# Kernel optimization log

Hardware: AMD Instinct MI355X
Metric: run time of the kernel (lower is better)

The kernel has to match this reference:

```python
import jax, jax.numpy as jnp
import numpy as np

HEADS = 4
DIM_HEAD = 32
SCALE = 10.0
EPS = 1e-12  # F.normalize eps


def setup_inputs() -> dict:
    key = jax.random.key(0)
    k0, k1, k2 = jax.random.split(key, 3)
    b, c, h, w = 4, 256, 64, 64
    hidden = HEADS * DIM_HEAD  # 128
    x = jax.random.normal(k0, (b, c, h, w), dtype=jnp.float32)
    # 1x1 convs == per-pixel linear layers; store as [out_ch, in_ch]
    w_qkv = jax.random.normal(k1, (3 * hidden, c), dtype=jnp.float32) * (1.0 / np.sqrt(c))
    w_out = jax.random.normal(k2, (c, hidden), dtype=jnp.float32) * (1.0 / np.sqrt(hidden))
    b_out = jnp.zeros((c,), dtype=jnp.float32)
    return {"x": x, "w_qkv": w_qkv, "w_out": w_out, "b_out": b_out}


def _l2norm(t):
    # normalize along the per-head feature dim d (axis=2 of [b,h,d,n])
    n = jnp.sqrt(jnp.sum(t * t, axis=2, keepdims=True))
    return t / jnp.maximum(n, EPS)


def reference(x, w_qkv, w_out, b_out):
    b, c, h, w = x.shape
    n = h * w
    # to_qkv 1x1 conv (no bias)
    qkv = jnp.einsum('oc,bchw->bohw', w_qkv, x)          # [b, 3*hidden, h, w]
    qkv = qkv.reshape(b, 3, HEADS, DIM_HEAD, n)          # chunk dim=1 then split heads
    q, k, v = qkv[:, 0], qkv[:, 1], qkv[:, 2]            # each [b, heads, d, n]
    q = _l2norm(q)
    k = _l2norm(k)
    sim = jnp.einsum('bhdi,bhdj->bhij', q, k) * SCALE    # [b, heads, n, n]
    attn = jax.nn.softmax(sim, axis=-1)
    out = jnp.einsum('bhij,bhdj->bhid', attn, v)         # [b, heads, n, d]
    # 'b h (x y) d -> b (h d) x y'
    out = out.transpose(0, 1, 3, 2).reshape(b, HEADS * DIM_HEAD, h, w)
    # to_out 1x1 conv with bias
    return jnp.einsum('oc,bchw->bohw', w_out, out) + b_out[None, :, None, None]
```

## Files before the change

### kernel.cpp

```cpp
#include <hip/hip_runtime.h>
#include <math.h>

#define BB 4
#define CC 256
#define NHEAD 4
#define DH 32
#define NN 4096
#define HID 128

typedef _Float16 f16;
typedef _Float16 f16x8 __attribute__((ext_vector_type(8)));
typedef _Float16 f16x4 __attribute__((ext_vector_type(4)));
typedef float f32x4 __attribute__((ext_vector_type(4)));

#define QPRESCALE 14.42695041f
#define NSHIFT 14.42695041f

#if __has_builtin(__builtin_amdgcn_exp2f)
#define EXP2F(x) __builtin_amdgcn_exp2f(x)
#else
#define EXP2F(x) __expf((x)*0.6931471805599453f)
#endif

__device__ __forceinline__ f16x8 cvt8(const float* p) {
    float4 a = *(const float4*)p;
    float4 b = *(const float4*)(p + 4);
    f16x8 r;
    r[0] = (f16)a.x; r[1] = (f16)a.y; r[2] = (f16)a.z; r[3] = (f16)a.w;
    r[4] = (f16)b.x; r[5] = (f16)b.y; r[6] = (f16)b.z; r[7] = (f16)b.w;
    return r;
}

__global__ __launch_bounds__(256) void qkv_fused(const float* __restrict__ x,
                                                 const float* __restrict__ wq,
                                                 f16* __restrict__ qh,
                                                 f16* __restrict__ kh,
                                                 f16* __restrict__ vh) {
    int wave = threadIdx.x >> 6, lane = threadIdx.x & 63;
    int quad = lane >> 4, col = lane & 15;
    int b = blockIdx.z;
    int o0 = blockIdx.y * 64;
    int i0 = blockIdx.x * 128 + wave * 32;
    const float* xb = x + (size_t)b * CC * NN;

    f32x4 c[4][2];
#pragma unroll
    for (int mt = 0; mt < 4; mt++)
#pragma unroll
        for (int nt = 0; nt < 2; nt++) c[mt][nt] = f32x4{0.f, 0.f, 0.f, 0.f};

#pragma unroll
    for (int k0 = 0; k0 < CC; k0 += 32) {
        f16x8 a[4];
#pragma unroll
        for (int mt = 0; mt < 4; mt++)
            a[mt] = cvt8(wq + (size_t)(o0 + mt * 16 + col) * CC + k0 + quad * 8);
#pragma unroll
        for (int nt = 0; nt < 2; nt++) {
            const float* xc = xb + (size_t)(k0 + quad * 8) * NN + i0 + nt * 16 + col;
            f16x8 bf;
#pragma unroll
            for (int j = 0; j < 8; j++) bf[j] = (f16)xc[(size_t)j * NN];
#pragma unroll
            for (int mt = 0; mt < 4; mt++)
                c[mt][nt] = __builtin_amdgcn_mfma_f32_16x16x32_f16(a[mt], bf, c[mt][nt], 0, 0, 0);
        }
    }

    if (o0 < 256) {
        int isQ = (o0 < 128);
        int obase = isQ ? o0 : (o0 - 128);
        f16* dst = isQ ? qh : kh;
        float pre = isQ ? QPRESCALE : 1.0f;
#pragma unroll
        for (int nt = 0; nt < 2; nt++) {
#pragma unroll
            for (int hh = 0; hh < 2; hh++) {
                float ss = 0.f;
#pragma unroll
                for (int m2 = 0; m2 < 2; m2++)
#pragma unroll
                    for (int r = 0; r < 4; r++) {
                        float v = c[hh * 2 + m2][nt][r];
                        ss = fmaf(v, v, ss);
                    }
                ss += __shfl_xor(ss, 16);
                ss += __shfl_xor(ss, 32);
                float inv = pre / fmaxf(sqrtf(ss), 1e-12f);
                int h = (obase + hh * 32) >> 5;
                size_t row = ((size_t)(b * 4 + h) * NN + i0 + nt * 16 + col) * 32;
#pragma unroll
                for (int m2 = 0; m2 < 2; m2++) {
                    f16x4 st;
#pragma unroll
                    for (int r = 0; r < 4; r++) st[r] = (f16)(c[hh * 2 + m2][nt][r] * inv);
                    *(f16x4*)(dst + row + m2 * 16 + quad * 4) = st;
                }
            }
        }
    } else {
        int o2 = o0 - 256;
#pragma unroll
        for (int nt = 0; nt < 2; nt++) {
            int i = i0 + nt * 16 + col;
#pragma unroll
            for (int mt = 0; mt < 4; mt++) {
                int h = (o2 + mt * 16) >> 5;
                int d = (mt & 1) * 16 + quad * 4;
#pragma unroll
                for (int r = 0; r < 4; r++)
                    vh[((size_t)(b * 4 + h) * 32 + d + r) * NN + i] = (f16)c[mt][nt][r];
            }
        }
    }
}

#define KROW 40
#define VROW 72

struct KV32 {
    f16x8 k0, k1;
    f16x4 v0n0, v0n1, v1n0, v1n1;
};

__device__ __forceinline__ KV32 lds_frags(const f16* kl, const f16* vl,
                                          int jb, int col, int quad) {
    KV32 f;
    f.k0 = *(const f16x8*)(kl + (jb + col) * KROW + quad * 8);
    f.k1 = *(const f16x8*)(kl + (jb + 16 + col) * KROW + quad * 8);
    f.v0n0 = *(const f16x4*)(vl + col * VROW + jb + quad * 4);
    f.v0n1 = *(const f16x4*)(vl + (16 + col) * VROW + jb + quad * 4);
    f.v1n0 = *(const f16x4*)(vl + col * VROW + jb + 16 + quad * 4);
    f.v1n1 = *(const f16x4*)(vl + (16 + col) * VROW + jb + 16 + quad * 4);
    return f;
}

__device__ __forceinline__ f16x4 expblk(f32x4 s, float& lacc) {
    float p0 = EXP2F(s[0]), p1 = EXP2F(s[1]);
    float p2 = EXP2F(s[2]), p3 = EXP2F(s[3]);
    lacc += (p0 + p1) + (p2 + p3);
    f16x4 r;
    r[0] = (f16)p0; r[1] = (f16)p1; r[2] = (f16)p2; r[3] = (f16)p3;
    return r;
}

__device__ __forceinline__ void compute32(const KV32& f, f16x8 qB0, f16x8 qB1,
                                          f32x4& o00, f32x4& o01,
                                          f32x4& o10, f32x4& o11,
                                          float& l0, float& l1) {
    const f32x4 zs = {-NSHIFT, -NSHIFT, -NSHIFT, -NSHIFT};
    f32x4 s00 = __builtin_amdgcn_mfma_f32_16x16x32_f16(f.k0, qB0, zs, 0, 0, 0);
    f32x4 s10 = __builtin_amdgcn_mfma_f32_16x16x32_f16(f.k0, qB1, zs, 0, 0, 0);
    f32x4 s01 = __builtin_amdgcn_mfma_f32_16x16x32_f16(f.k1, qB0, zs, 0, 0, 0);
    f32x4 s11 = __builtin_amdgcn_mfma_f32_16x16x32_f16(f.k1, qB1, zs, 0, 0, 0);
    f16x4 p00 = expblk(s00, l0);
    f16x4 p10 = expblk(s10, l1);
    f16x4 p01 = expblk(s01, l0);
    f16x4 p11 = expblk(s11, l1);
    o00 = __builtin_amdgcn_mfma_f32_16x16x16f16(p00, f.v0n0, o00, 0, 0, 0);
    o01 = __builtin_amdgcn_mfma_f32_16x16x16f16(p00, f.v0n1, o01, 0, 0, 0);
    o10 = __builtin_amdgcn_mfma_f32_16x16x16f16(p10, f.v0n0, o10, 0, 0, 0);
    o11 = __builtin_amdgcn_mfma_f32_16x16x16f16(p10, f.v0n1, o11, 0, 0, 0);
    o00 = __builtin_amdgcn_mfma_f32_16x16x16f16(p01, f.v1n0, o00, 0, 0, 0);
    o01 = __builtin_amdgcn_mfma_f32_16x16x16f16(p01, f.v1n1, o01, 0, 0, 0);
    o10 = __builtin_amdgcn_mfma_f32_16x16x16f16(p11, f.v1n0, o10, 0, 0, 0);
    o11 = __builtin_amdgcn_mfma_f32_16x16x16f16(p11, f.v1n1, o11, 0, 0, 0);
}

__global__ __launch_bounds__(256, 4) void attn_mfma(const f16* __restrict__ qh,
                                                    const f16* __restrict__ kh,
                                                    const f16* __restrict__ vh,
                                                    f16* __restrict__ att16) {
    __shared__ __align__(16) f16 klds[2][64 * KROW];
    __shared__ __align__(16) f16 vlds[2][32 * VROW];
    int t = threadIdx.x;
    int wave = t >> 6, lane = t & 63;
    int quad = lane >> 4, col = lane & 15;

    int bid = blockIdx.x;
    int xcd = bid & 7;
    int slot = bid >> 3;
    int bh = xcd * 2 + (slot >> 5);
    int i0 = (slot & 31) * 128;
    int iw = i0 + wave * 32;

    const f16* qb = qh + (size_t)bh * NN * 32;
    const f16* kb = kh + (size_t)bh * NN * 32;
    const f16* vb = vh + (size_t)bh * 32 * NN;

    f16x8 qB0 = *(const f16x8*)(qb + (size_t)(iw + col) * 32 + quad * 8);
    f16x8 qB1 = *(const f16x8*)(qb + (size_t)(iw + 16 + col) * 32 + quad * 8);

    f32x4 o00 = {0.f, 0.f, 0.f, 0.f}, o01 = o00, o10 = o00, o11 = o00;
    float l0 = 0.f, l1 = 0.f;

    int ktr = t >> 2, kts = t & 3;
    int vtr = t >> 3, vts = t & 7;

    f16x8 kr, vr;
    kr = *(const f16x8*)(kb + (size_t)(0 + ktr) * 32 + kts * 8);
    vr = *(const f16x8*)(vb + (size_t)vtr * NN + 0 + vts * 8);
    *(f16x8*)(&klds[0][0] + ktr * KROW + kts * 8) = kr;
    *(f16x8*)(&vlds[0][0] + vtr * VROW + vts * 8) = vr;
    __syncthreads();
    kr = *(const f16x8*)(kb + (size_t)(64 + ktr) * 32 + kts * 8);
    vr = *(const f16x8*)(vb + (size_t)vtr * NN + 64 + vts * 8);

    for (int tile = 0; tile < 62; tile++) {
        int buf = tile & 1;
        const f16* kl = &klds[buf][0];
        const f16* vl = &vlds[buf][0];
        KV32 f0 = lds_frags(kl, vl, 0, col, quad);
        KV32 f1 = lds_frags(kl, vl, 32, col, quad);
        compute32(f0, qB0, qB1, o00, o01, o10, o11, l0, l1);
        compute32(f1, qB0, qB1, o00, o01, o10, o11, l0, l1);
        *(f16x8*)(&klds[buf ^ 1][0] + ktr * KROW + kts * 8) = kr;
        *(f16x8*)(&vlds[buf ^ 1][0] + vtr * VROW + vts * 8) = vr;
        __syncthreads();
        int j0 = (tile + 2) * 64;
        kr = *(const f16x8*)(kb + (size_t)(j0 + ktr) * 32 + kts * 8);
        vr = *(const f16x8*)(vb + (size_t)vtr * NN + j0 + vts * 8);
    }
    {
        KV32 f0 = lds_frags(&klds[0][0], &vlds[0][0], 0, col, quad);
        KV32 f1 = lds_frags(&klds[0][0], &vlds[0][0], 32, col, quad);
        compute32(f0, qB0, qB1, o00, o01, o10, o11, l0, l1);
        compute32(f1, qB0, qB1, o00, o01, o10, o11, l0, l1);
        *(f16x8*)(&klds[1][0] + ktr * KROW + kts * 8) = kr;
        *(f16x8*)(&vlds[1][0] + vtr * VROW + vts * 8) = vr;
        __syncthreads();
    }
    {
        KV32 f0 = lds_frags(&klds[1][0], &vlds[1][0], 0, col, quad);
        KV32 f1 = lds_frags(&klds[1][0], &vlds[1][0], 32, col, quad);
        compute32(f0, qB0, qB1, o00, o01, o10, o11, l0, l1);
        compute32(f1, qB0, qB1, o00, o01, o10, o11, l0, l1);
    }

    l0 += __shfl_xor(l0, 16); l0 += __shfl_xor(l0, 32);
    l1 += __shfl_xor(l1, 16); l1 += __shfl_xor(l1, 32);

    int b = bh >> 2, h = bh & 3;
    f16* ab = att16 + (size_t)b * NN * HID + h * 32;
#pragma unroll
    for (int r = 0; r < 4; r++) {
        float inv0 = __builtin_amdgcn_rcpf(__shfl(l0, quad * 4 + r));
        float inv1 = __builtin_amdgcn_rcpf(__shfl(l1, quad * 4 + r));
        size_t row0 = (size_t)(iw + quad * 4 + r) * HID;
        size_t row1 = (size_t)(iw + 16 + quad * 4 + r) * HID;
        ab[row0 + col]      = (f16)(o00[r] * inv0);
        ab[row0 + 16 + col] = (f16)(o01[r] * inv0);
        ab[row1 + col]      = (f16)(o10[r] * inv1);
        ab[row1 + 16 + col] = (f16)(o11[r] * inv1);
    }
}

__global__ __launch_bounds__(256) void out_mfma(const f16* __restrict__ att16,
                                                const float* __restrict__ wo,
                                                const float* __restrict__ bo,
                                                float* __restrict__ out) {
    int wave = threadIdx.x >> 6, lane = threadIdx.x & 63;
    int quad = lane >> 4, col = lane & 15;
    int b = blockIdx.z;
    int i0 = (blockIdx.x * 4 + wave) * 32;
    int o0 = blockIdx.y * 64;
    const f16* ab = att16 + (size_t)b * NN * HID;

    const f32x4 z = {0.f, 0.f, 0.f, 0.f};
    f32x4 c[2][4];
#pragma unroll
    for (int it = 0; it < 2; it++)
#pragma unroll
        for (int ot = 0; ot < 4; ot++) c[it][ot] = z;

#pragma unroll
    for (int k0 = 0; k0 < HID; k0 += 32) {
        f16x8 a0 = *(const f16x8*)(ab + (size_t)(i0 + col) * HID + k0 + quad * 8);
        f16x8 a1 = *(const f16x8*)(ab + (size_t)(i0 + 16 + col) * HID + k0 + quad * 8);
#pragma unroll
        for (int ot = 0; ot < 4; ot++) {
            f16x8 bf = cvt8(wo + (size_t)(o0 + ot * 16 + col) * HID + k0 + quad * 8);
            c[0][ot] = __builtin_amdgcn_mfma_f32_16x16x32_f16(a0, bf, c[0][ot], 0, 0, 0);
            c[1][ot] = __builtin_amdgcn_mfma_f32_16x16x32_f16(a1, bf, c[1][ot], 0, 0, 0);
        }
    }

#pragma unroll
    for (int it = 0; it < 2; it++)
#pragma unroll
        for (int ot = 0; ot < 4; ot++) {
            int o = o0 + ot * 16 + col;
            float bias = bo[o];
            int i = i0 + it * 16 + quad * 4;
            float4 st = {c[it][ot][0] + bias, c[it][ot][1] + bias,
                         c[it][ot][2] + bias, c[it][ot][3] + bias};
            *(float4*)(out + ((size_t)b * CC + o) * NN + i) = st;
        }
}

extern "C" void kernel_launch(void* const* d_in, const int* in_sizes, int n_in,
                              void* d_out, int out_size, void* d_ws, size_t ws_size,
                              hipStream_t stream) {
    const float* x     = (const float*)d_in[0];
    const float* w_qkv = (const float*)d_in[1];
    const float* w_out = (const float*)d_in[2];
    const float* b_out = (const float*)d_in[3];
    float* out = (float*)d_out;

    char* ws = (char*)d_ws;
    f16* qh    = (f16*)(ws);
    f16* kh    = (f16*)(ws + (4u << 20));
    f16* vh    = (f16*)(ws + (8u << 20));
    f16* att16 = (f16*)(ws + (12u << 20));

    qkv_fused<<<dim3(NN / 128, 384 / 64, BB), 256, 0, stream>>>(x, w_qkv, qh, kh, vh);
    attn_mfma<<<dim3(512), 256, 0, stream>>>(qh, kh, vh, att16);
    out_mfma<<<dim3(NN / 128, CC / 64, BB), 256, 0, stream>>>(att16, w_out, b_out, out);
}
```

Baseline: 167.8 us.

## Retile attention to 16 queries per wave and widen output tiles in projections

The attention kernel now gives each wave 16 query rows instead of 32 and launches 1024 blocks instead of 512. This spreads the dominant attention work over more CUs, but each block reloads the full K/V stream for half as many queries. The QKV and output projection kernels double the output channels per block (128 instead of 64), so each x or att16 fragment load feeds more MFMAs. The cost is more accumulator registers and fewer blocks in those two kernels.

```diff
diff --git a/kernel.cpp b/kernel.cpp
--- a/kernel.cpp
+++ b/kernel.cpp
@@ -39,43 +39,41 @@
     int wave = threadIdx.x >> 6, lane = threadIdx.x & 63;
     int quad = lane >> 4, col = lane & 15;
     int b = blockIdx.z;
-    int o0 = blockIdx.y * 64;
+    int y = blockIdx.y;
+    int o0 = y * 128;
     int i0 = blockIdx.x * 128 + wave * 32;
     const float* xb = x + (size_t)b * CC * NN;
 
-    f32x4 c[4][2];
-#pragma unroll
-    for (int mt = 0; mt < 4; mt++)
+    f32x4 c[8][2];
+#pragma unroll
+    for (int mt = 0; mt < 8; mt++)
 #pragma unroll
         for (int nt = 0; nt < 2; nt++) c[mt][nt] = f32x4{0.f, 0.f, 0.f, 0.f};
 
 #pragma unroll
     for (int k0 = 0; k0 < CC; k0 += 32) {
-        f16x8 a[4];
-#pragma unroll
-        for (int mt = 0; mt < 4; mt++)
-            a[mt] = cvt8(wq + (size_t)(o0 + mt * 16 + col) * CC + k0 + quad * 8);
+        f16x8 bf[2];
 #pragma unroll
         for (int nt = 0; nt < 2; nt++) {
             const float* xc = xb + (size_t)(k0 + quad * 8) * NN + i0 + nt * 16 + col;
-            f16x8 bf;
-#pragma unroll
-            for (int j = 0; j < 8; j++) bf[j] = (f16)xc[(size_t)j * NN];
-#pragma unroll
-            for (int mt = 0; mt < 4; mt++)
-                c[mt][nt] = __builtin_amdgcn_mfma_f32_16x16x32_f16(a[mt], bf, c[mt][nt], 0, 0, 0);
-        }
-    }
-
-    if (o0 < 256) {
-        int isQ = (o0 < 128);
-        int obase = isQ ? o0 : (o0 - 128);
-        f16* dst = isQ ? qh : kh;
-        float pre = isQ ? QPRESCALE : 1.0f;
+#pragma unroll
+            for (int j = 0; j < 8; j++) bf[nt][j] = (f16)xc[(size_t)j * NN];
+        }
+#pragma unroll
+        for (int mt = 0; mt < 8; mt++) {
+            f16x8 a = cvt8(wq + (size_t)(o0 + mt * 16 + col) * CC + k0 + quad * 8);
+            c[mt][0] = __builtin_amdgcn_mfma_f32_16x16x32_f16(a, bf[0], c[mt][0], 0, 0, 0);
+            c[mt][1] = __builtin_amdgcn_mfma_f32_16x16x32_f16(a, bf[1], c[mt][1], 0, 0, 0);
+        }
+    }
+
+    if (y < 2) {
+        f16* dst = (y == 0) ? qh : kh;
+        float pre = (y == 0) ? QPRESCALE : 1.0f;
 #pragma unroll
         for (int nt = 0; nt < 2; nt++) {
 #pragma unroll
-            for (int hh = 0; hh < 2; hh++) {
+            for (int hh = 0; hh < 4; hh++) {
                 float ss = 0.f;
 #pragma unroll
                 for (int m2 = 0; m2 < 2; m2++)
@@ -87,8 +85,7 @@
                 ss += __shfl_xor(ss, 16);
                 ss += __shfl_xor(ss, 32);
                 float inv = pre / fmaxf(sqrtf(ss), 1e-12f);
-                int h = (obase + hh * 32) >> 5;
-                size_t row = ((size_t)(b * 4 + h) * NN + i0 + nt * 16 + col) * 32;
+                size_t row = ((size_t)(b * 4 + hh) * NN + i0 + nt * 16 + col) * 32;
 #pragma unroll
                 for (int m2 = 0; m2 < 2; m2++) {
                     f16x4 st;
@@ -99,13 +96,12 @@
             }
         }
     } else {
-        int o2 = o0 - 256;
 #pragma unroll
         for (int nt = 0; nt < 2; nt++) {
             int i = i0 + nt * 16 + col;
 #pragma unroll
-            for (int mt = 0; mt < 4; mt++) {
-                int h = (o2 + mt * 16) >> 5;
+            for (int mt = 0; mt < 8; mt++) {
+                int h = mt >> 1;
                 int d = (mt & 1) * 16 + quad * 4;
 #pragma unroll
                 for (int r = 0; r < 4; r++)
@@ -144,27 +140,17 @@
     return r;
 }
 
-__device__ __forceinline__ void compute32(const KV32& f, f16x8 qB0, f16x8 qB1,
-                                          f32x4& o00, f32x4& o01,
-                                          f32x4& o10, f32x4& o11,
-                                          float& l0, float& l1) {
+__device__ __forceinline__ void compute16(const KV32& f, f16x8 qB0,
+                                          f32x4& o00, f32x4& o01, float& l0) {
     const f32x4 zs = {-NSHIFT, -NSHIFT, -NSHIFT, -NSHIFT};
-    f32x4 s00 = __builtin_amdgcn_mfma_f32_16x16x32_f16(f.k0, qB0, zs, 0, 0, 0);
-    f32x4 s10 = __builtin_amdgcn_mfma_f32_16x16x32_f16(f.k0, qB1, zs, 0, 0, 0);
-    f32x4 s01 = __builtin_amdgcn_mfma_f32_16x16x32_f16(f.k1, qB0, zs, 0, 0, 0);
-    f32x4 s11 = __builtin_amdgcn_mfma_f32_16x16x32_f16(f.k1, qB1, zs, 0, 0, 0);
-    f16x4 p00 = expblk(s00, l0);
-    f16x4 p10 = expblk(s10, l1);
-    f16x4 p01 = expblk(s01, l0);
-    f16x4 p11 = expblk(s11, l1);
-    o00 = __builtin_amdgcn_mfma_f32_16x16x16f16(p00, f.v0n0, o00, 0, 0, 0);
-    o01 = __builtin_amdgcn_mfma_f32_16x16x16f16(p00, f.v0n1, o01, 0, 0, 0);
-    o10 = __builtin_amdgcn_mfma_f32_16x16x16f16(p10, f.v0n0, o10, 0, 0, 0);
-    o11 = __builtin_amdgcn_mfma_f32_16x16x16f16(p10, f.v0n1, o11, 0, 0, 0);
-    o00 = __builtin_amdgcn_mfma_f32_16x16x16f16(p01, f.v1n0, o00, 0, 0, 0);
-    o01 = __builtin_amdgcn_mfma_f32_16x16x16f16(p01, f.v1n1, o01, 0, 0, 0);
-    o10 = __builtin_amdgcn_mfma_f32_16x16x16f16(p11, f.v1n0, o10, 0, 0, 0);
-    o11 = __builtin_amdgcn_mfma_f32_16x16x16f16(p11, f.v1n1, o11, 0, 0, 0);
+    f32x4 s0 = __builtin_amdgcn_mfma_f32_16x16x32_f16(f.k0, qB0, zs, 0, 0, 0);
+    f32x4 s1 = __builtin_amdgcn_mfma_f32_16x16x32_f16(f.k1, qB0, zs, 0, 0, 0);
+    f16x4 p0 = expblk(s0, l0);
+    f16x4 p1 = expblk(s1, l0);
+    o00 = __builtin_amdgcn_mfma_f32_16x16x16f16(p0, f.v0n0, o00, 0, 0, 0);
+    o01 = __builtin_amdgcn_mfma_f32_16x16x16f16(p0, f.v0n1, o01, 0, 0, 0);
+    o00 = __builtin_amdgcn_mfma_f32_16x16x16f16(p1, f.v1n0, o00, 0, 0, 0);
+    o01 = __builtin_amdgcn_mfma_f32_16x16x16f16(p1, f.v1n1, o01, 0, 0, 0);
 }
 
 __global__ __launch_bounds__(256, 4) void attn_mfma(const f16* __restrict__ qh,
@@ -180,19 +166,18 @@
     int bid = blockIdx.x;
     int xcd = bid & 7;
     int slot = bid >> 3;
-    int bh = xcd * 2 + (slot >> 5);
-    int i0 = (slot & 31) * 128;
-    int iw = i0 + wave * 32;
+    int bh = xcd * 2 + (slot >> 6);
+    int i0 = (slot & 63) * 64;
+    int iw = i0 + wave * 16;
 
     const f16* qb = qh + (size_t)bh * NN * 32;
     const f16* kb = kh + (size_t)bh * NN * 32;
     const f16* vb = vh + (size_t)bh * 32 * NN;
 
     f16x8 qB0 = *(const f16x8*)(qb + (size_t)(iw + col) * 32 + quad * 8);
-    f16x8 qB1 = *(const f16x8*)(qb + (size_t)(iw + 16 + col) * 32 + quad * 8);
-
-    f32x4 o00 = {0.f, 0.f, 0.f, 0.f}, o01 = o00, o10 = o00, o11 = o00;
-    float l0 = 0.f, l1 = 0.f;
+
+    f32x4 o00 = {0.f, 0.f, 0.f, 0.f}, o01 = o00;
+    float l0 = 0.f;
 
     int ktr = t >> 2, kts = t & 3;
     int vtr = t >> 3, vts = t & 7;
@@ -212,8 +197,8 @@
         const f16* vl = &vlds[buf][0];
         KV32 f0 = lds_frags(kl, vl, 0, col, quad);
         KV32 f1 = lds_frags(kl, vl, 32, col, quad);
-        compute32(f0, qB0, qB1, o00, o01, o10, o11, l0, l1);
-        compute32(f1, qB0, qB1, o00, o01, o10, o11, l0, l1);
+        compute16(f0, qB0, o00, o01, l0);
+        compute16(f1, qB0, o00, o01, l0);
         *(f16x8*)(&klds[buf ^ 1][0] + ktr * KROW + kts * 8) = kr;
         *(f16x8*)(&vlds[buf ^ 1][0] + vtr * VROW + vts * 8) = vr;
         __syncthreads();
@@ -224,8 +209,8 @@
     {
         KV32 f0 = lds_frags(&klds[0][0], &vlds[0][0], 0, col, quad);
         KV32 f1 = lds_frags(&klds[0][0], &vlds[0][0], 32, col, quad);
-        compute32(f0, qB0, qB1, o00, o01, o10, o11, l0, l1);
-        compute32(f1, qB0, qB1, o00, o01, o10, o11, l0, l1);
+        compute16(f0, qB0, o00, o01, l0);
+        compute16(f1, qB0, o00, o01, l0);
         *(f16x8*)(&klds[1][0] + ktr * KROW + kts * 8) = kr;
         *(f16x8*)(&vlds[1][0] + vtr * VROW + vts * 8) = vr;
         __syncthreads();
@@ -233,25 +218,20 @@
     {
         KV32 f0 = lds_frags(&klds[1][0], &vlds[1][0], 0, col, quad);
         KV32 f1 = lds_frags(&klds[1][0], &vlds[1][0], 32, col, quad);
-        compute32(f0, qB0, qB1, o00, o01, o10, o11, l0, l1);
-        compute32(f1, qB0, qB1, o00, o01, o10, o11, l0, l1);
+        compute16(f0, qB0, o00, o01, l0);
+        compute16(f1, qB0, o00, o01, l0);
     }
 
     l0 += __shfl_xor(l0, 16); l0 += __shfl_xor(l0, 32);
-    l1 += __shfl_xor(l1, 16); l1 += __shfl_xor(l1, 32);
 
     int b = bh >> 2, h = bh & 3;
     f16* ab = att16 + (size_t)b * NN * HID + h * 32;
 #pragma unroll
     for (int r = 0; r < 4; r++) {
         float inv0 = __builtin_amdgcn_rcpf(__shfl(l0, quad * 4 + r));
-        float inv1 = __builtin_amdgcn_rcpf(__shfl(l1, quad * 4 + r));
         size_t row0 = (size_t)(iw + quad * 4 + r) * HID;
-        size_t row1 = (size_t)(iw + 16 + quad * 4 + r) * HID;
         ab[row0 + col]      = (f16)(o00[r] * inv0);
         ab[row0 + 16 + col] = (f16)(o01[r] * inv0);
-        ab[row1 + col]      = (f16)(o10[r] * inv1);
-        ab[row1 + 16 + col] = (f16)(o11[r] * inv1);
     }
 }
 
@@ -263,22 +243,21 @@
     int quad = lane >> 4, col = lane & 15;
     int b = blockIdx.z;
     int i0 = (blockIdx.x * 4 + wave) * 32;
-    int o0 = blockIdx.y * 64;
+    int o0 = blockIdx.y * 128;
     const f16* ab = att16 + (size_t)b * NN * HID;
 
-    const f32x4 z = {0.f, 0.f, 0.f, 0.f};
-    f32x4 c[2][4];
+    f32x4 c[2][8];
 #pragma unroll
     for (int it = 0; it < 2; it++)
 #pragma unroll
-        for (int ot = 0; ot < 4; ot++) c[it][ot] = z;
+        for (int ot = 0; ot < 8; ot++) c[it][ot] = f32x4{0.f, 0.f, 0.f, 0.f};
 
 #pragma unroll
     for (int k0 = 0; k0 < HID; k0 += 32) {
         f16x8 a0 = *(const f16x8*)(ab + (size_t)(i0 + col) * HID + k0 + quad * 8);
         f16x8 a1 = *(const f16x8*)(ab + (size_t)(i0 + 16 + col) * HID + k0 + quad * 8);
 #pragma unroll
-        for (int ot = 0; ot < 4; ot++) {
+        for (int ot = 0; ot < 8; ot++) {
             f16x8 bf = cvt8(wo + (size_t)(o0 + ot * 16 + col) * HID + k0 + quad * 8);
             c[0][ot] = __builtin_amdgcn_mfma_f32_16x16x32_f16(a0, bf, c[0][ot], 0, 0, 0);
             c[1][ot] = __builtin_amdgcn_mfma_f32_16x16x32_f16(a1, bf, c[1][ot], 0, 0, 0);
@@ -288,7 +267,7 @@
 #pragma unroll
     for (int it = 0; it < 2; it++)
 #pragma unroll
-        for (int ot = 0; ot < 4; ot++) {
+        for (int ot = 0; ot < 8; ot++) {
             int o = o0 + ot * 16 + col;
             float bias = bo[o];
             int i = i0 + it * 16 + quad * 4;
@@ -313,7 +292,7 @@
     f16* vh    = (f16*)(ws + (8u << 20));
     f16* att16 = (f16*)(ws + (12u << 20));
 
-    qkv_fused<<<dim3(NN / 128, 384 / 64, BB), 256, 0, stream>>>(x, w_qkv, qh, kh, vh);
-    attn_mfma<<<dim3(512), 256, 0, stream>>>(qh, kh, vh, att16);
-    out_mfma<<<dim3(NN / 128, CC / 64, BB), 256, 0, stream>>>(att16, w_out, b_out, out);
-}
+    qkv_fused<<<dim3(NN / 128, 3, BB), 256, 0, stream>>>(x, w_qkv, qh, kh, vh);
+    attn_mfma<<<dim3(1024), 256, 0, stream>>>(qh, kh, vh, att16);
+    out_mfma<<<dim3(NN / 128, 2, BB), 256, 0, stream>>>(att16, w_out, b_out, out);
+}
```

Measured after the change: 181.9 us. 1.08x slower.
